# Kernel tuning notes

Measured on AMD Instinct MI355X. Metric: run time of the kernel, lower is better.

Reference implementation:

```python
import jax, jax.numpy as jnp
import numpy as np

S, HID, H, D, G = 2048, 4096, 32, 128, 2   # seq, hidden, heads, head_dim, kv groups
ROT = D // 2                               # rotary applied to first half of head_dim
QKV = HID + 2 * G * D                      # 4608


def setup_inputs() -> dict:
    key = jax.random.key(0)
    k1, k2, k3 = jax.random.split(key, 3)
    sc = 0.02
    return {
        "hidden_states": jax.random.normal(k1, (S, HID), jnp.float32),
        "W_qkv": jax.random.normal(k2, (HID, QKV), jnp.float32) * sc,
        "b_qkv": jnp.zeros((QKV,), jnp.float32),
        "W_dense": jax.random.normal(k3, (HID, HID), jnp.float32) * sc,
    }


def _rope(x, pos):
    # x: [S, n_heads, ROT]; interleaved-pair rotation (ChatGLM2 convention)
    half = ROT // 2
    inv_freq = 10000.0 ** (-jnp.arange(0, ROT, 2, dtype=jnp.float32) / ROT)  # [half]
    theta = pos[:, None] * inv_freq                                          # [S, half]
    cos = jnp.cos(theta)[:, None, :]
    sin = jnp.sin(theta)[:, None, :]
    xp = x.reshape(x.shape[0], x.shape[1], half, 2)
    x0, x1 = xp[..., 0], xp[..., 1]
    out = jnp.stack([x0 * cos - x1 * sin, x1 * cos + x0 * sin], axis=-1)
    return out.reshape(x.shape)


def reference(hidden_states, W_qkv, b_qkv, W_dense):
    qkv = hidden_states @ W_qkv + b_qkv            # [S, QKV]
    q = qkv[:, : H * D].reshape(S, H, D)           # [S, H, D]
    k = qkv[:, H * D : H * D + G * D].reshape(S, G, D)
    v = qkv[:, H * D + G * D :].reshape(S, G, D)

    pos = jnp.arange(S, dtype=jnp.float32)
    q = jnp.concatenate([_rope(q[..., :ROT], pos), q[..., ROT:]], axis=-1)
    k = jnp.concatenate([_rope(k[..., :ROT], pos), k[..., ROT:]], axis=-1)

    gidx = jnp.arange(H) % G                       # head -> kv group (MQA/GQA)
    kh = k[:, gidx, :]                             # [S, H, D]
    vh = v[:, gidx, :]

    scores = jnp.einsum('shd,thd->hst', q, kh) / jnp.sqrt(jnp.float32(D))
    causal = jnp.tril(jnp.ones((S, S), bool))
    scores = jnp.where(causal[None], scores, jnp.float32(-1e9))
    p = jax.nn.softmax(scores, axis=-1)            # [H, S, S]
    ctx = jnp.einsum('hst,thd->shd', p, vh).reshape(S, HID)
    return ctx @ W_dense
```

## Files before the change

kernel.cpp:

```cpp
#include <hip/hip_runtime.h>
#include <hip/hip_bf16.h>

#define S_LEN 2048
#define HIDN  4096
#define NH    32
#define HD    128
#define QKV_N 4608
#define K_OFF 4096
#define V_OFF 4352
#define SCALE 0.08838834764831845f

typedef __attribute__((ext_vector_type(8))) short   short8;
typedef __attribute__((ext_vector_type(4))) float   f32x4;
typedef __attribute__((ext_vector_type(4))) unsigned short ushort4v;
typedef __attribute__((ext_vector_type(8))) unsigned short ushort8;

typedef __attribute__((address_space(1))) const unsigned int GU32;
typedef __attribute__((address_space(3))) unsigned int LU32;

__device__ __forceinline__ void async16(const void* g, void* l) {
  __builtin_amdgcn_global_load_lds((GU32*)g, (LU32*)l, 16, 0, 0);
}

__device__ __forceinline__ unsigned short f2bf(float x) {
  __hip_bfloat16 h = __float2bfloat16(x);
  return *reinterpret_cast<unsigned short*>(&h);
}
__device__ __forceinline__ float bf2f(unsigned short u) {
  __hip_bfloat16 h = *reinterpret_cast<__hip_bfloat16*>(&u);
  return __bfloat162float(h);
}

__global__ void k_cvt_bf16(const float* __restrict__ in, unsigned short* __restrict__ out, int n4) {
  int i = blockIdx.x * 256 + threadIdx.x;
  if (i >= n4) return;
  const float4 v = reinterpret_cast<const float4*>(in)[i];
  ushort4v o = { f2bf(v.x), f2bf(v.y), f2bf(v.z), f2bf(v.w) };
  reinterpret_cast<ushort4v*>(out)[i] = o;
}

__global__ __launch_bounds__(256) void k_transpose_cvt(const float* __restrict__ W,
                                                       unsigned short* __restrict__ WT,
                                                       int K, int N) {
  __shared__ float tl[64][65];
  const int n0 = blockIdx.x * 64, k0 = blockIdx.y * 64;
  const int t = threadIdx.x;
  const int r = t >> 4, c4 = (t & 15) << 2;
#pragma unroll
  for (int p = 0; p < 4; ++p) {
    int krow = p * 16 + r;
    const float4 v = *reinterpret_cast<const float4*>(&W[(size_t)(k0 + krow) * N + n0 + c4]);
    tl[krow][c4 + 0] = v.x; tl[krow][c4 + 1] = v.y;
    tl[krow][c4 + 2] = v.z; tl[krow][c4 + 3] = v.w;
  }
  __syncthreads();
#pragma unroll
  for (int p = 0; p < 4; ++p) {
    int nrow = p * 16 + r;
    ushort4v o = { f2bf(tl[c4 + 0][nrow]), f2bf(tl[c4 + 1][nrow]),
                   f2bf(tl[c4 + 2][nrow]), f2bf(tl[c4 + 3][nrow]) };
    *reinterpret_cast<ushort4v*>(&WT[(size_t)(n0 + nrow) * K + k0 + c4]) = o;
  }
}

template <int BIAS, int OUTBF>
__global__ __launch_bounds__(256, 2) void k_gemm_bt(const unsigned short* __restrict__ A,
                                                    const unsigned short* __restrict__ Bt,
                                                    const float* __restrict__ bias,
                                                    void* __restrict__ Cout,
                                                    int M, int N, int K) {
  __shared__ __align__(16) unsigned char lds[32768];
  const int tid = threadIdx.x;
  const int l = tid & 63, w = tid >> 6;
  const int wr = w >> 1, wc = w & 1;
  const int l16 = l & 15, lh = l >> 4;
  const int nx = N >> 7;
  const int cpx = gridDim.x >> 3;
  const int wg = (blockIdx.x & 7) * cpx + (blockIdx.x >> 3);
  const int m0 = (wg / nx) * 128, n0 = (wg % nx) * 128;
  const size_t rowK = (size_t)K * 2;
  const char* Ab = (const char*)A + (size_t)m0 * rowK;
  const char* Bb = (const char*)Bt + (size_t)n0 * rowK;
  f32x4 acc[4][4] = {};
  const int nkt = K >> 6;
  for (int kt = 0; kt < nkt; ++kt) {
    const int kbyte = kt << 7;
#pragma unroll
    for (int rr = 0; rr < 4; ++rr) {
      int off = rr * 4096 + tid * 16;
      int row = off >> 7;
      int col = (off & 127) ^ ((row & 7) << 4);
      async16(Ab + (size_t)row * rowK + kbyte + col, lds + off);
    }
#pragma unroll
    for (int rr = 0; rr < 4; ++rr) {
      int off = rr * 4096 + tid * 16;
      int row = off >> 7;
      int col = (off & 127) ^ ((row & 7) << 4);
      async16(Bb + (size_t)row * rowK + kbyte + col, lds + 16384 + off);
    }
    __syncthreads();
#pragma unroll
    for (int kk = 0; kk < 2; ++kk) {
      short8 af[4], bfr[4];
#pragma unroll
      for (int m = 0; m < 4; ++m) {
        int arow = wr * 64 + m * 16 + l16;
        int byte = (arow << 7) + kk * 64 + lh * 16;
        byte ^= (arow & 7) << 4;
        af[m] = *reinterpret_cast<const short8*>(lds + byte);
      }
#pragma unroll
      for (int n = 0; n < 4; ++n) {
        int brow = wc * 64 + n * 16 + l16;
        int byte = (brow << 7) + kk * 64 + lh * 16;
        byte ^= (brow & 7) << 4;
        bfr[n] = *reinterpret_cast<const short8*>(lds + 16384 + byte);
      }
#pragma unroll
      for (int m = 0; m < 4; ++m)
#pragma unroll
        for (int n = 0; n < 4; ++n)
          acc[m][n] = __builtin_amdgcn_mfma_f32_16x16x32_bf16(af[m], bfr[n], acc[m][n], 0, 0, 0);
    }
    __syncthreads();
  }
#pragma unroll
  for (int m = 0; m < 4; ++m) {
    int grow = m0 + wr * 64 + m * 16 + lh * 4;
#pragma unroll
    for (int n = 0; n < 4; ++n) {
      int gcol = n0 + wc * 64 + n * 16 + l16;
      float bv = BIAS ? bias[gcol] : 0.f;
      f32x4 v = acc[m][n];
#pragma unroll
      for (int j = 0; j < 4; ++j) {
        float val = v[j] + bv;
        if (OUTBF) ((unsigned short*)Cout)[(size_t)(grow + j) * N + gcol] = f2bf(val);
        else       ((float*)Cout)[(size_t)(grow + j) * N + gcol] = val;
      }
    }
  }
}

__global__ void k_rope(unsigned short* __restrict__ qkv) {
  const int p = blockIdx.x * 64 + threadIdx.x;
  const int s = blockIdx.y;
  const int i = p & 31;
  const int hh = p >> 5;
  const int col = (hh < 32) ? (hh * HD + 2 * i) : (K_OFF + (hh - 32) * HD + 2 * i);
  unsigned int* ptr = (unsigned int*)(qkv + (size_t)s * QKV_N + col);
  unsigned int both = *ptr;
  float x0 = bf2f((unsigned short)(both & 0xffffu));
  float x1 = bf2f((unsigned short)(both >> 16));
  float inv = expf(-0.28782313662425572f * (float)i);
  float theta = (float)s * inv;
  float sn, cs;
  sincosf(theta, &sn, &cs);
  float y0 = x0 * cs - x1 * sn;
  float y1 = x1 * cs + x0 * sn;
  *ptr = (unsigned int)f2bf(y0) | ((unsigned int)f2bf(y1) << 16);
}

__global__ __launch_bounds__(256) void k_transpose_v(const unsigned short* __restrict__ qkv,
                                                     unsigned short* __restrict__ Vt) {
  __shared__ __align__(16) unsigned short tl[64][72];
  const int st = blockIdx.x * 64;
  const int dt = blockIdx.y * 64;
  const int g = blockIdx.z;
  const int t = threadIdx.x;
  const int r = t >> 3;
  const int seg = (t & 7) * 8;
#pragma unroll
  for (int p = 0; p < 2; ++p) {
    int srow = p * 32 + r;
    ushort8 v = *reinterpret_cast<const ushort8*>(
        &qkv[(size_t)(st + srow) * QKV_N + V_OFF + g * HD + dt + seg]);
    *reinterpret_cast<ushort8*>(&tl[srow][seg]) = v;
  }
  __syncthreads();
#pragma unroll
  for (int p = 0; p < 2; ++p) {
    int drow = p * 32 + r;
    ushort8 o;
#pragma unroll
    for (int i = 0; i < 8; ++i) o[i] = tl[seg + i][drow];
    *reinterpret_cast<ushort8*>(&Vt[((size_t)g * HD + dt + drow) * S_LEN + st + seg]) = o;
  }
}

__device__ __forceinline__ void stage_kv(const char* Kb, const char* Vb,
                                         unsigned char* ldsK, unsigned char* ldsV, int tid) {
  __builtin_amdgcn_sched_barrier(0);
#pragma unroll
  for (int rr = 0; rr < 4; ++rr) {
    int off = rr * 4096 + tid * 16;
    int row = off >> 8;
    int col = (off & 255) ^ ((row & 15) << 4);
    async16(Kb + (size_t)row * (QKV_N * 2) + col, ldsK + off);
  }
#pragma unroll
  for (int rr = 0; rr < 4; ++rr) {
    int off = rr * 4096 + tid * 16;
    int row = off >> 7;
    int col = (off & 127) ^ ((row & 7) << 4);
    async16(Vb + (size_t)row * (S_LEN * 2) + col, ldsV + off);
  }
  __builtin_amdgcn_sched_barrier(0);
}

__global__ __launch_bounds__(256) void k_attn(const unsigned short* __restrict__ qkv,
                                              const unsigned short* __restrict__ Vt,
                                              unsigned short* __restrict__ ctx) {
  __shared__ __align__(16) unsigned char lds[73728];
  const int tid = threadIdx.x;
  const int l = tid & 63, w = tid >> 6;
  const int l16 = l & 15, lh = l >> 4;
  const int h = blockIdx.y;
  const int g = h & 1;
  const int b = blockIdx.x;
  const int tA = 31 - b;
  const int nA = tA + 1;
  const int nT = nA + b + 1;
  const int q0A = tA * 64, q0B = b * 64;

  const char* Kbase = (const char*)(qkv + K_OFF + g * HD);
  const char* Vbase = (const char*)(Vt + ((size_t)g * HD) * S_LEN);

  short8 vones;
#pragma unroll
  for (int e = 0; e < 8; ++e) vones[e] = (short)0x3F80;

  short8 qf[4];
#pragma unroll
  for (int ks = 0; ks < 4; ++ks)
    qf[ks] = *reinterpret_cast<const short8*>(
        qkv + (size_t)(q0A + w * 16 + l16) * QKV_N + h * HD + ks * 32 + lh * 8);

  f32x4 o[8] = {};
  f32x4 lacc = {};
  float m_run = -1e30f;

  stage_kv(Kbase, Vbase, lds, lds + 32768, tid);

  for (int it = 0; it < nT; ++it) {
    const int phase = (it >= nA) ? 1 : 0;
    const int kt = phase ? (it - nA) : it;
    const int q0 = phase ? q0B : q0A;
    const int k0 = kt << 6;
    const int nxt = it + 1;
    if (nxt < nT) {
      const int kn = ((nxt >= nA) ? (nxt - nA) : nxt) << 6;
      stage_kv(Kbase + (size_t)kn * (QKV_N * 2), Vbase + (size_t)kn * 2,
               lds + (nxt & 1) * 16384, lds + 32768 + (nxt & 1) * 16384, tid);
      asm volatile("s_waitcnt vmcnt(8)" ::: "memory");
    } else {
      asm volatile("s_waitcnt vmcnt(0)" ::: "memory");
    }
    __builtin_amdgcn_s_barrier();
    __builtin_amdgcn_sched_barrier(0);

    const unsigned char* Kl = lds + (it & 1) * 16384;
    const unsigned char* Vl = lds + 32768 + (it & 1) * 16384;

    f32x4 sf[4] = {};
    __builtin_amdgcn_s_setprio(1);
#pragma unroll
    for (int n = 0; n < 4; ++n) {
      int krow = n * 16 + l16;
      int swz = (krow & 15) << 4;
#pragma unroll
      for (int ks = 0; ks < 4; ++ks) {
        int byte = (krow << 8) + ks * 64 + lh * 16;
        short8 kf = *reinterpret_cast<const short8*>(Kl + (byte ^ swz));
        sf[n] = __builtin_amdgcn_mfma_f32_16x16x32_bf16(qf[ks], kf, sf[n], 0, 0, 0);
      }
    }
    __builtin_amdgcn_s_setprio(0);

    const int qrow0 = q0 + w * 16 + lh * 4;
    float tmax = -1e30f;
#pragma unroll
    for (int n = 0; n < 4; ++n) {
      int key = k0 + n * 16 + l16;
#pragma unroll
      for (int j = 0; j < 4; ++j) {
        float v = sf[n][j] * SCALE;
        v = (key <= qrow0 + j) ? v : -1e30f;
        sf[n][j] = v;
        tmax = fmaxf(tmax, v);
      }
    }
#pragma unroll
    for (int d = 1; d < 64; d <<= 1) tmax = fmaxf(tmax, __shfl_xor(tmax, d, 64));
    if (tmax > m_run + 8.f) {
      float fsc = __expf(m_run - tmax);
      m_run = tmax;
#pragma unroll
      for (int n8 = 0; n8 < 8; ++n8) o[n8] *= fsc;
      lacc *= fsc;
    }

    unsigned char* Pb = lds + 65536 + w * 2048;
#pragma unroll
    for (int n = 0; n < 4; ++n)
#pragma unroll
      for (int j = 0; j < 4; ++j) {
        int row = lh * 4 + j;
        int byte = (row << 7) + (n * 16 + l16) * 2;
        byte ^= (row & 7) << 4;
        *(unsigned short*)(Pb + byte) = f2bf(__expf(sf[n][j] - m_run));
      }

    __builtin_amdgcn_s_setprio(1);
#pragma unroll
    for (int kk = 0; kk < 2; ++kk) {
      int pbyte = (l16 << 7) + kk * 64 + lh * 16;
      pbyte ^= (l16 & 7) << 4;
      short8 pa = *reinterpret_cast<const short8*>(Pb + pbyte);
      lacc = __builtin_amdgcn_mfma_f32_16x16x32_bf16(pa, vones, lacc, 0, 0, 0);
#pragma unroll
      for (int n8 = 0; n8 < 8; ++n8) {
        int vrow = n8 * 16 + l16;
        int vbyte = (vrow << 7) + kk * 64 + lh * 16;
        vbyte ^= (vrow & 7) << 4;
        short8 vb = *reinterpret_cast<const short8*>(Vl + vbyte);
        o[n8] = __builtin_amdgcn_mfma_f32_16x16x32_bf16(pa, vb, o[n8], 0, 0, 0);
      }
    }
    __builtin_amdgcn_s_setprio(0);

    if (it == nA - 1) {
#pragma unroll
      for (int n8 = 0; n8 < 8; ++n8) {
        int col = h * HD + n8 * 16 + l16;
#pragma unroll
        for (int j = 0; j < 4; ++j) {
          int row = q0A + w * 16 + lh * 4 + j;
          ctx[(size_t)row * HIDN + col] = f2bf(o[n8][j] / lacc[j]);
        }
      }
#pragma unroll
      for (int n8 = 0; n8 < 8; ++n8) o[n8] = f32x4{0.f, 0.f, 0.f, 0.f};
      lacc = f32x4{0.f, 0.f, 0.f, 0.f};
      m_run = -1e30f;
      __builtin_amdgcn_sched_barrier(0);
#pragma unroll
      for (int ks = 0; ks < 4; ++ks)
        qf[ks] = *reinterpret_cast<const short8*>(
            qkv + (size_t)(q0B + w * 16 + l16) * QKV_N + h * HD + ks * 32 + lh * 8);
      __builtin_amdgcn_sched_barrier(0);
    }
    __builtin_amdgcn_s_barrier();
  }

#pragma unroll
  for (int n8 = 0; n8 < 8; ++n8) {
    int col = h * HD + n8 * 16 + l16;
#pragma unroll
    for (int j = 0; j < 4; ++j) {
      int row = q0B + w * 16 + lh * 4 + j;
      ctx[(size_t)row * HIDN + col] = f2bf(o[n8][j] / lacc[j]);
    }
  }
}

extern "C" void kernel_launch(void* const* d_in, const int* in_sizes, int n_in,
                              void* d_out, int out_size, void* d_ws, size_t ws_size,
                              hipStream_t stream) {
  const float* hidden = (const float*)d_in[0];
  const float* Wqkv = (const float*)d_in[1];
  const float* bqkv = (const float*)d_in[2];
  const float* Wd = (const float*)d_in[3];
  char* ws = (char*)d_ws;
  unsigned short* hid_bf = (unsigned short*)(ws);
  unsigned short* WqkvT  = (unsigned short*)(ws + 16777216);
  unsigned short* WdT    = (unsigned short*)(ws + 54525952);
  unsigned short* qkv    = (unsigned short*)(ws + 88080384);
  unsigned short* Vt     = (unsigned short*)(ws + 106954752);
  unsigned short* ctx    = (unsigned short*)(ws + 108003328);

  k_cvt_bf16<<<8192, 256, 0, stream>>>(hidden, hid_bf, 2097152);
  k_transpose_cvt<<<dim3(72, 64), 256, 0, stream>>>(Wqkv, WqkvT, 4096, 4608);
  k_transpose_cvt<<<dim3(64, 64), 256, 0, stream>>>(Wd, WdT, 4096, 4096);
  k_gemm_bt<1, 1><<<576, 256, 0, stream>>>(hid_bf, WqkvT, bqkv, qkv, 2048, 4608, 4096);
  k_rope<<<dim3(17, 2048), 64, 0, stream>>>(qkv);
  k_transpose_v<<<dim3(32, 2, 2), 256, 0, stream>>>(qkv, Vt);
  k_attn<<<dim3(16, 32), 256, 0, stream>>>(qkv, Vt, ctx);
  k_gemm_bt<0, 0><<<512, 256, 0, stream>>>(ctx, WdT, nullptr, d_out, 2048, 4096, 4096);
}
```

Measured before the change: 301.6 us.

## Load V fragments directly from global memory instead of staging through LDS

```diff
diff --git a/kernel.cpp b/kernel.cpp
--- a/kernel.cpp
+++ b/kernel.cpp
@@ -64,11 +64,11 @@
 }
 
 template <int BIAS, int OUTBF>
-__global__ __launch_bounds__(256, 2) void k_gemm_bt(const unsigned short* __restrict__ A,
-                                                    const unsigned short* __restrict__ Bt,
-                                                    const float* __restrict__ bias,
-                                                    void* __restrict__ Cout,
-                                                    int M, int N, int K) {
+__global__ __launch_bounds__(256) void k_gemm_bt(const unsigned short* __restrict__ A,
+                                                 const unsigned short* __restrict__ Bt,
+                                                 const float* __restrict__ bias,
+                                                 void* __restrict__ Cout,
+                                                 int M, int N, int K) {
   __shared__ __align__(16) unsigned char lds[32768];
   const int tid = threadIdx.x;
   const int l = tid & 63, w = tid >> 6;
@@ -189,8 +189,7 @@
   }
 }
 
-__device__ __forceinline__ void stage_kv(const char* Kb, const char* Vb,
-                                         unsigned char* ldsK, unsigned char* ldsV, int tid) {
+__device__ __forceinline__ void stage_k(const char* Kb, unsigned char* ldsK, int tid) {
   __builtin_amdgcn_sched_barrier(0);
 #pragma unroll
   for (int rr = 0; rr < 4; ++rr) {
@@ -199,20 +198,13 @@
     int col = (off & 255) ^ ((row & 15) << 4);
     async16(Kb + (size_t)row * (QKV_N * 2) + col, ldsK + off);
   }
-#pragma unroll
-  for (int rr = 0; rr < 4; ++rr) {
-    int off = rr * 4096 + tid * 16;
-    int row = off >> 7;
-    int col = (off & 127) ^ ((row & 7) << 4);
-    async16(Vb + (size_t)row * (S_LEN * 2) + col, ldsV + off);
-  }
   __builtin_amdgcn_sched_barrier(0);
 }
 
 __global__ __launch_bounds__(256) void k_attn(const unsigned short* __restrict__ qkv,
                                               const unsigned short* __restrict__ Vt,
                                               unsigned short* __restrict__ ctx) {
-  __shared__ __align__(16) unsigned char lds[73728];
+  __shared__ __align__(16) unsigned char lds[40960];
   const int tid = threadIdx.x;
   const int l = tid & 63, w = tid >> 6;
   const int l16 = l & 15, lh = l >> 4;
@@ -225,7 +217,7 @@
   const int q0A = tA * 64, q0B = b * 64;
 
   const char* Kbase = (const char*)(qkv + K_OFF + g * HD);
-  const char* Vbase = (const char*)(Vt + ((size_t)g * HD) * S_LEN);
+  const unsigned short* Vgl = Vt + (size_t)g * HD * S_LEN;
 
   short8 vones;
 #pragma unroll
@@ -241,7 +233,7 @@
   f32x4 lacc = {};
   float m_run = -1e30f;
 
-  stage_kv(Kbase, Vbase, lds, lds + 32768, tid);
+  stage_k(Kbase, lds, tid);
 
   for (int it = 0; it < nT; ++it) {
     const int phase = (it >= nA) ? 1 : 0;
@@ -251,9 +243,8 @@
     const int nxt = it + 1;
     if (nxt < nT) {
       const int kn = ((nxt >= nA) ? (nxt - nA) : nxt) << 6;
-      stage_kv(Kbase + (size_t)kn * (QKV_N * 2), Vbase + (size_t)kn * 2,
-               lds + (nxt & 1) * 16384, lds + 32768 + (nxt & 1) * 16384, tid);
-      asm volatile("s_waitcnt vmcnt(8)" ::: "memory");
+      stage_k(Kbase + (size_t)kn * (QKV_N * 2), lds + (nxt & 1) * 16384, tid);
+      asm volatile("s_waitcnt vmcnt(4)" ::: "memory");
     } else {
       asm volatile("s_waitcnt vmcnt(0)" ::: "memory");
     }
@@ -261,7 +252,6 @@
     __builtin_amdgcn_sched_barrier(0);
 
     const unsigned char* Kl = lds + (it & 1) * 16384;
-    const unsigned char* Vl = lds + 32768 + (it & 1) * 16384;
 
     f32x4 sf[4] = {};
     __builtin_amdgcn_s_setprio(1);
@@ -301,7 +291,7 @@
       lacc *= fsc;
     }
 
-    unsigned char* Pb = lds + 65536 + w * 2048;
+    unsigned char* Pb = lds + 32768 + w * 2048;
 #pragma unroll
     for (int n = 0; n < 4; ++n)
 #pragma unroll
@@ -319,13 +309,18 @@
       pbyte ^= (l16 & 7) << 4;
       short8 pa = *reinterpret_cast<const short8*>(Pb + pbyte);
       lacc = __builtin_amdgcn_mfma_f32_16x16x32_bf16(pa, vones, lacc, 0, 0, 0);
-#pragma unroll
-      for (int n8 = 0; n8 < 8; ++n8) {
-        int vrow = n8 * 16 + l16;
-        int vbyte = (vrow << 7) + kk * 64 + lh * 16;
-        vbyte ^= (vrow & 7) << 4;
-        short8 vb = *reinterpret_cast<const short8*>(Vl + vbyte);
-        o[n8] = __builtin_amdgcn_mfma_f32_16x16x32_bf16(pa, vb, o[n8], 0, 0, 0);
+      const unsigned short* vcol = Vgl + k0 + kk * 32 + lh * 8;
+#pragma unroll
+      for (int half = 0; half < 2; ++half) {
+        short8 vb[4];
+#pragma unroll
+        for (int q = 0; q < 4; ++q) {
+          int n8 = half * 4 + q;
+          vb[q] = *reinterpret_cast<const short8*>(vcol + (size_t)(n8 * 16 + l16) * S_LEN);
+        }
+#pragma unroll
+        for (int q = 0; q < 4; ++q)
+          o[half * 4 + q] = __builtin_amdgcn_mfma_f32_16x16x32_bf16(pa, vb[q], o[half * 4 + q], 0, 0, 0);
       }
     }
     __builtin_amdgcn_s_setprio(0);
```

Measured after the change: 421.6 us. 1.4x slower.
